# Kernel tuning notes

Hardware: AMD Instinct MI355X
Metric: run time of the kernel (lower is better)

Reference implementation:

```python
import jax, jax.numpy as jnp
import numpy as np

B, S, HID = 8, 1024, 1024
NH, HD = 16, 64  # num heads, head dim; NH*HD == HID


def setup_inputs() -> dict:
    key = jax.random.key(0)
    ks = jax.random.split(key, 8)
    sc = 0.02
    return {
        "hidden_states": jax.random.normal(ks[0], (B, S, HID), jnp.float32),
        "attention_mask": jnp.zeros((B, 1, 1, S), jnp.float32),
        "Wq": jax.random.normal(ks[1], (HID, HID), jnp.float32) * sc,
        "bq": jnp.zeros((HID,), jnp.float32),
        "Wk": jax.random.normal(ks[2], (HID, HID), jnp.float32) * sc,
        "bk": jnp.zeros((HID,), jnp.float32),
        "Wv": jax.random.normal(ks[3], (HID, HID), jnp.float32) * sc,
        "bv": jnp.zeros((HID,), jnp.float32),
    }


def reference(hidden_states, attention_mask, Wq, bq, Wk, bk, Wv, bv):
    def split_heads(x):  # [B,S,HID] -> [B,NH,S,HD]
        return x.reshape(B, S, NH, HD).transpose(0, 2, 1, 3)

    q = split_heads(hidden_states @ Wq + bq)
    k = split_heads(hidden_states @ Wk + bk)
    v = split_heads(hidden_states @ Wv + bv)

    # [B,NH,S,S] score matrix, scale, additive mask, softmax
    scores = jnp.einsum("bhqd,bhkd->bhqk", q, k) / jnp.sqrt(jnp.float32(HD))
    scores = scores + attention_mask
    probs = jax.nn.softmax(scores, axis=-1)  # dropout prob = 0.0 -> identity

    ctx = jnp.einsum("bhqk,bhkd->bhqd", probs, v)
    return ctx.transpose(0, 2, 1, 3).reshape(B, S, HID)
```

## Files before the change

### kernel.cpp

```cpp
#include <hip/hip_runtime.h>


typedef __bf16 bf16x8 __attribute__((ext_vector_type(8)));
typedef float f32x4 __attribute__((ext_vector_type(4)));
typedef float f32x16 __attribute__((ext_vector_type(16)));

__device__ __forceinline__ unsigned rne16(float x) {
  unsigned u = __builtin_bit_cast(unsigned, x);
  return (u + 0x7fffu + ((u >> 16) & 1u)) >> 16;
}
__device__ __forceinline__ unsigned packbf(float lo, float hi) {
  return rne16(lo) | (rne16(hi) << 16);
}
__device__ __forceinline__ unsigned packbf_fast(float lo, float hi) {
  unsigned ul = __builtin_bit_cast(unsigned, lo) + 0x8000u;
  unsigned uh = __builtin_bit_cast(unsigned, hi) + 0x8000u;
  return __builtin_amdgcn_perm(uh, ul, 0x07060302u);
}
__device__ __forceinline__ void async16(void* l, const void* g) {
  __builtin_amdgcn_global_load_lds((const __attribute__((address_space(1))) void*)g,
                                   (__attribute__((address_space(3))) void*)l, 16, 0, 0);
}

__global__ __launch_bounds__(256) void k_prep(const float* __restrict__ h,
                                              unsigned short* __restrict__ hbf,
                                              const float* __restrict__ Wq,
                                              const float* __restrict__ Wk,
                                              const float* __restrict__ Wv,
                                              unsigned short* __restrict__ wt) {
  __shared__ float t[32][33];
  int bid = blockIdx.x, tid = threadIdx.x;
  if (bid < 8192) {
    size_t i = (size_t)bid * 256 + tid;
    float4 v = ((const float4*)h)[i];
    uint2 r;
    r.x = packbf(v.x, v.y);
    r.y = packbf(v.z, v.w);
    ((uint2*)hbf)[i] = r;
  } else {
    int id = bid - 8192;
    int which = id >> 10;
    int sub = id & 1023;
    int c0 = (sub & 31) * 32, k0 = (sub >> 5) * 32;
    const float* W = which == 0 ? Wq : (which == 1 ? Wk : Wv);
    int tx = tid & 31, ty = tid >> 5;
#pragma unroll
    for (int i = 0; i < 4; ++i) {
      int r = ty + i * 8;
      t[r][tx] = W[(size_t)(k0 + r) * 1024 + c0 + tx];
    }
    __syncthreads();
#pragma unroll
    for (int i = 0; i < 4; ++i) {
      int r = ty + i * 8;
      wt[((size_t)which * 1024 + c0 + r) * 1024 + k0 + tx] = (unsigned short)rne16(t[tx][r]);
    }
  }
}

__global__ __launch_bounds__(256, 2) void k_gemm(const unsigned short* __restrict__ A,
                                                 const unsigned short* __restrict__ Bm,
                                                 const float* __restrict__ bq,
                                                 const float* __restrict__ bk,
                                                 const float* __restrict__ bv,
                                                 unsigned short* __restrict__ qkv,
                                                 unsigned short* __restrict__ vt) {
  __shared__ __align__(16) char lds[65536];
  const int tid = threadIdx.x;
  const int w = tid >> 6, lane = tid & 63;
  const int wm = w >> 1, wn = w & 1;

  int orig = blockIdx.x;
  int wgid = (orig & 7) * 192 + (orig >> 3);
  int tm = wgid / 24, tn = wgid - tm * 24;
  int m0 = tm * 128, n0 = tn * 128;

  int ro[4], ke[4];
#pragma unroll
  for (int j = 0; j < 4; ++j) {
    int o = j * 4096 + tid * 16;
    int s = o >> 10, w10 = o & 1023;
    int lg = w10 ^ (((w10 >> 9) & 1) << 5);
    ro[j] = ((s >> 1) << 4) + (lg >> 6);
    ke[j] = ((s & 1) << 5) + ((lg & 63) >> 1);
  }
  auto stage = [&](int kt, char* buf) {
    const unsigned short* As = A + (size_t)m0 * 1024 + kt * 64;
    const unsigned short* Bs = Bm + (size_t)n0 * 1024 + kt * 64;
#pragma unroll
    for (int j = 0; j < 4; ++j) {
      async16(buf + j * 4096 + tid * 16, As + (size_t)ro[j] * 1024 + ke[j]);
      async16(buf + 16384 + j * 4096 + tid * 16, Bs + (size_t)ro[j] * 1024 + ke[j]);
    }
  };

  const int lswz = (((lane & 15) << 6) | ((lane >> 4) << 4)) ^ ((lane & 8) << 2);

  f32x4 acc[4][4];
#pragma unroll
  for (int i = 0; i < 4; ++i)
#pragma unroll
    for (int j = 0; j < 4; ++j)
#pragma unroll
      for (int e = 0; e < 4; ++e) acc[i][j][e] = 0.f;

  auto compute = [&](const char* buf) {
    const char* abase = buf + lswz;
    const char* bbase = buf + 16384 + lswz;
#pragma unroll
    for (int ks = 0; ks < 2; ++ks) {
      bf16x8 bF[4];
#pragma unroll
      for (int n = 0; n < 4; ++n)
        bF[n] = *(const bf16x8*)(bbase + ((size_t)((wn * 4 + n) * 2 + ks) << 10));
#pragma unroll
      for (int mt = 0; mt < 4; ++mt) {
        bf16x8 a = *(const bf16x8*)(abase + ((size_t)((wm * 4 + mt) * 2 + ks) << 10));
#pragma unroll
        for (int n = 0; n < 4; ++n)
          acc[mt][n] =
              __builtin_amdgcn_mfma_f32_16x16x32_bf16(a, bF[n], acc[mt][n], 0, 0, 0);
      }
    }
  };

  char* buf0 = lds;
  char* buf1 = lds + 32768;
  stage(0, buf0);
#pragma unroll 1
  for (int kt = 0; kt < 16; kt += 2) {
    __syncthreads();
    stage(kt + 1, buf1);
    compute(buf0);
    __syncthreads();
    if (kt + 2 < 16) stage(kt + 2, buf0);
    compute(buf1);
  }

  const int which = tn >> 3;
  const int ng = n0 & 1023;
  const int b = m0 >> 10;
  const int r = lane & 15, qq = lane >> 4;
  const int sb = (m0 & 1023) + wm * 64 + qq * 4;

  if (which != 2) {
    const float* bp = which == 0 ? bq : bk;
    unsigned short* base = qkv + ((size_t)which << 23) + ((size_t)b << 20);
#pragma unroll
    for (int n = 0; n < 4; ++n) {
      int n_in = ng + wn * 64 + n * 16 + r;
      float bias = bp[n_in];
      unsigned short* dp = base + ((size_t)(n_in >> 6) << 16) + (n_in & 63);
#pragma unroll
      for (int m = 0; m < 4; ++m)
#pragma unroll
        for (int e = 0; e < 4; ++e)
          dp[(size_t)(sb + m * 16 + e) << 6] = (unsigned short)rne16(acc[m][n][e] + bias);
    }
  } else {
    unsigned short* vbase = vt + ((size_t)b << 20);
#pragma unroll
    for (int n = 0; n < 4; ++n) {
      int n_in = ng + wn * 64 + n * 16 + r;
      float bias = bv[n_in];
      unsigned short* dp = vbase + ((size_t)n_in << 10) + sb;
#pragma unroll
      for (int m = 0; m < 4; ++m) {
        uint2 pk;
        pk.x = packbf(acc[m][n][0] + bias, acc[m][n][1] + bias);
        pk.y = packbf(acc[m][n][2] + bias, acc[m][n][3] + bias);
        *(uint2*)(dp + m * 16) = pk;
      }
    }
  }
}

__global__ __launch_bounds__(256, 2) void k_attn(const unsigned short* __restrict__ qg,
                                                 const unsigned short* __restrict__ kg,
                                                 const unsigned short* __restrict__ vtg,
                                                 const float* __restrict__ maskg,
                                                 float* __restrict__ out) {
  __shared__ __align__(16) char lds[36864];
  float* MK = (float*)(lds + 32768);
  int tid = threadIdx.x, w = tid >> 6, lane = tid & 63, l5 = lane & 31, q5 = lane >> 5;
  int idx = blockIdx.x;
  int bi = idx & 7;
  int j = idx >> 3;
  int h = j >> 2, qc = j & 3;
  int bh = bi * 16 + h, s0 = qc * 256;
  const unsigned short* qb = qg + ((size_t)bh << 16);
  const unsigned short* kb = kg + ((size_t)bh << 16);
  const unsigned short* vb = vtg + ((size_t)bh << 16);
  const float LG = 1.4426950408889634f;
  const float C1 = 0.125f * LG;

  {
    float4 mv = *(const float4*)(maskg + (size_t)bi * 1024 + tid * 4);
    mv.x *= LG; mv.y *= LG; mv.z *= LG; mv.w *= LG;
    *(float4*)(MK + tid * 4) = mv;
  }

  auto stageKV = [&](int kt, char* buf) {
    int k0 = kt * 64;
#pragma unroll
    for (int t = 0; t < 2; ++t) {
      int f = w * 2 + t;
      int mt = f >> 2, ds = f & 3;
      async16(buf + f * 1024, kb + (size_t)(k0 + mt * 32 + l5) * 64 + ds * 16 + q5 * 8);
      int dt = f >> 2, ks = f & 3;
      async16(buf + 8192 + f * 1024,
              vb + (size_t)(dt * 32 + l5) * 1024 + k0 + ks * 16 + q5 * 8);
    }
  };

  bf16x8 qfr[2][4];
#pragma unroll
  for (int qh = 0; qh < 2; ++qh)
#pragma unroll
    for (int ds = 0; ds < 4; ++ds)
      qfr[qh][ds] = *(const bf16x8*)(qb + (size_t)(s0 + w * 64 + qh * 32 + l5) * 64 +
                                     ds * 16 + q5 * 8);

  f32x16 O[2][2];
#pragma unroll
  for (int qh = 0; qh < 2; ++qh)
#pragma unroll
    for (int i = 0; i < 2; ++i)
#pragma unroll
      for (int e = 0; e < 16; ++e) O[qh][i][e] = 0.f;
  float lsum0 = 0.f, lsum1 = 0.f;

  stageKV(0, lds);
  __syncthreads();

#pragma unroll 1
  for (int kt = 0; kt < 16; ++kt) {
    char* buf = lds + (kt & 1) * 16384;
    if (kt < 15) stageKV(kt + 1, lds + ((kt + 1) & 1) * 16384);
    int k0 = kt * 64;
    const char* KF = buf;
    const char* VF = buf + 8192;
#pragma unroll
    for (int mt = 0; mt < 2; ++mt) {
      f32x16 S0, S1;
#pragma unroll
      for (int e = 0; e < 16; ++e) { S0[e] = 0.f; S1[e] = 0.f; }
#pragma unroll
      for (int ds = 0; ds < 4; ++ds) {
        bf16x8 a = *(const bf16x8*)(KF + (mt * 4 + ds) * 1024 + lane * 16);
        S0 = __builtin_amdgcn_mfma_f32_32x32x16_bf16(a, qfr[0][ds], S0, 0, 0, 0);
        S1 = __builtin_amdgcn_mfma_f32_32x32x16_bf16(a, qfr[1][ds], S1, 0, 0, 0);
      }
      unsigned p2a[8], p2b[8];
      {
        float p[16];
#pragma unroll
        for (int g4 = 0; g4 < 4; ++g4) {
          float4 mv = *(const float4*)(MK + k0 + mt * 32 + g4 * 8 + q5 * 4);
          p[g4 * 4 + 0] = __builtin_amdgcn_exp2f(S0[g4 * 4 + 0] * C1 + mv.x);
          p[g4 * 4 + 1] = __builtin_amdgcn_exp2f(S0[g4 * 4 + 1] * C1 + mv.y);
          p[g4 * 4 + 2] = __builtin_amdgcn_exp2f(S0[g4 * 4 + 2] * C1 + mv.z);
          p[g4 * 4 + 3] = __builtin_amdgcn_exp2f(S0[g4 * 4 + 3] * C1 + mv.w);
        }
#pragma unroll
        for (int e = 0; e < 16; ++e) lsum0 += p[e];
#pragma unroll
        for (int jj = 0; jj < 8; ++jj) p2a[jj] = packbf_fast(p[2 * jj], p[2 * jj + 1]);
      }
      {
        float p[16];
#pragma unroll
        for (int g4 = 0; g4 < 4; ++g4) {
          float4 mv = *(const float4*)(MK + k0 + mt * 32 + g4 * 8 + q5 * 4);
          p[g4 * 4 + 0] = __builtin_amdgcn_exp2f(S1[g4 * 4 + 0] * C1 + mv.x);
          p[g4 * 4 + 1] = __builtin_amdgcn_exp2f(S1[g4 * 4 + 1] * C1 + mv.y);
          p[g4 * 4 + 2] = __builtin_amdgcn_exp2f(S1[g4 * 4 + 2] * C1 + mv.z);
          p[g4 * 4 + 3] = __builtin_amdgcn_exp2f(S1[g4 * 4 + 3] * C1 + mv.w);
        }
#pragma unroll
        for (int e = 0; e < 16; ++e) lsum1 += p[e];
#pragma unroll
        for (int jj = 0; jj < 8; ++jj) p2b[jj] = packbf_fast(p[2 * jj], p[2 * jj + 1]);
      }
#pragma unroll
      for (int kh = 0; kh < 2; ++kh) {
        int ks = mt * 2 + kh, gp = kh * 4;
        bf16x8 av0 = *(const bf16x8*)(VF + (0 * 4 + ks) * 1024 + lane * 16);
        bf16x8 av1 = *(const bf16x8*)(VF + (1 * 4 + ks) * 1024 + lane * 16);
        {
          unsigned o0 = p2a[gp + 0], o1 = p2a[gp + 1];
          unsigned o2 = p2a[gp + 2], o3 = p2a[gp + 3];
          unsigned t0 = __shfl_xor((int)o0, 32);
          unsigned t1 = __shfl_xor((int)o1, 32);
          unsigned t2 = __shfl_xor((int)o2, 32);
          unsigned t3 = __shfl_xor((int)o3, 32);
          uint4 fu;
          fu.x = q5 ? t2 : o0;
          fu.y = q5 ? t3 : o1;
          fu.z = q5 ? o2 : t0;
          fu.w = q5 ? o3 : t1;
          bf16x8 bfrag = __builtin_bit_cast(bf16x8, fu);
          O[0][0] = __builtin_amdgcn_mfma_f32_32x32x16_bf16(av0, bfrag, O[0][0], 0, 0, 0);
          O[0][1] = __builtin_amdgcn_mfma_f32_32x32x16_bf16(av1, bfrag, O[0][1], 0, 0, 0);
        }
        {
          unsigned o0 = p2b[gp + 0], o1 = p2b[gp + 1];
          unsigned o2 = p2b[gp + 2], o3 = p2b[gp + 3];
          unsigned t0 = __shfl_xor((int)o0, 32);
          unsigned t1 = __shfl_xor((int)o1, 32);
          unsigned t2 = __shfl_xor((int)o2, 32);
          unsigned t3 = __shfl_xor((int)o3, 32);
          uint4 fu;
          fu.x = q5 ? t2 : o0;
          fu.y = q5 ? t3 : o1;
          fu.z = q5 ? o2 : t0;
          fu.w = q5 ? o3 : t1;
          bf16x8 bfrag = __builtin_bit_cast(bf16x8, fu);
          O[1][0] = __builtin_amdgcn_mfma_f32_32x32x16_bf16(av0, bfrag, O[1][0], 0, 0, 0);
          O[1][1] = __builtin_amdgcn_mfma_f32_32x32x16_bf16(av1, bfrag, O[1][1], 0, 0, 0);
        }
      }
    }
    __syncthreads();
  }

  float* Ob = (float*)(lds + w * 8192);
  float lt0 = lsum0 + __shfl_xor(lsum0, 32);
  float lt1 = lsum1 + __shfl_xor(lsum1, 32);
  float rinv0 = 1.0f / lt0;
  float rinv1 = 1.0f / lt1;
#pragma unroll
  for (int qh = 0; qh < 2; ++qh) {
    float rinv = qh ? rinv1 : rinv0;
#pragma unroll
    for (int dt = 0; dt < 2; ++dt)
#pragma unroll
      for (int g4 = 0; g4 < 4; ++g4) {
        float4 val;
        val.x = O[qh][dt][g4 * 4 + 0] * rinv;
        val.y = O[qh][dt][g4 * 4 + 1] * rinv;
        val.z = O[qh][dt][g4 * 4 + 2] * rinv;
        val.w = O[qh][dt][g4 * 4 + 3] * rinv;
        int c = dt * 8 + g4 * 2 + q5;
        *(float4*)(Ob + l5 * 64 + (c ^ (l5 & 15)) * 4) = val;
      }
#pragma unroll
    for (int t = 0; t < 8; ++t) {
      int qr = t * 4 + (lane >> 4), cr = lane & 15;
      float4 vv = *(const float4*)(Ob + qr * 64 + (cr ^ (qr & 15)) * 4);
      int s = s0 + w * 64 + qh * 32 + qr;
      *(float4*)(out + (((size_t)(bi * 1024 + s)) << 10) + (h << 6) + (cr << 2)) = vv;
    }
  }
}

extern "C" void kernel_launch(void* const* d_in, const int* in_sizes, int n_in,
                              void* d_out, int out_size, void* d_ws, size_t ws_size,
                              hipStream_t stream) {
  (void)in_sizes; (void)n_in; (void)out_size; (void)ws_size;
  const float* hidden = (const float*)d_in[0];
  const float* mask = (const float*)d_in[1];
  const float* Wq = (const float*)d_in[2];
  const float* bq = (const float*)d_in[3];
  const float* Wk = (const float*)d_in[4];
  const float* bk = (const float*)d_in[5];
  const float* Wv = (const float*)d_in[6];
  const float* bv = (const float*)d_in[7];
  float* out = (float*)d_out;
  char* ws = (char*)d_ws;
  unsigned short* hbf = (unsigned short*)ws;
  unsigned short* wt  = (unsigned short*)(ws + 16777216);
  unsigned short* qkv = (unsigned short*)(ws + 23068672);
  unsigned short* vt  = (unsigned short*)(ws + 56623104);

  k_prep<<<11264, 256, 0, stream>>>(hidden, hbf, Wq, Wk, Wv, wt);
  k_gemm<<<1536, 256, 0, stream>>>(hbf, wt, bq, bk, bv, qkv, vt);
  k_attn<<<512, 256, 0, stream>>>(qkv, qkv + 8388608, vt, mask, out);
}
```

Measured before the change: 209.0 us.

## Widen QKV GEMM tiles to 128x384 with half-depth K stages

Reshapes the fused QKV projection GEMM from 128x128 tiles to 128x384 tiles, so each workgroup covers three times as many output columns and reuses its A tile across them. The K step per stage is halved to 32 so the LDS buffers still fit, and the grid drops from 1536 to 512 workgroups. Each wave now holds 48 accumulator fragments, which raises register pressure and may force spills or lower occupancy. The smaller grid also gives fewer workgroups per CU for hiding latency.

```diff
diff --git a/kernel.cpp b/kernel.cpp
--- a/kernel.cpp
+++ b/kernel.cpp
@@ -71,56 +71,54 @@
   const int wm = w >> 1, wn = w & 1;
 
   int orig = blockIdx.x;
-  int wgid = (orig & 7) * 192 + (orig >> 3);
-  int tm = wgid / 24, tn = wgid - tm * 24;
-  int m0 = tm * 128, n0 = tn * 128;
-
-  int ro[4], ke[4];
-#pragma unroll
-  for (int j = 0; j < 4; ++j) {
+  int wgid = (orig & 7) * 64 + (orig >> 3);
+  int tm = wgid >> 3, tn = wgid & 7;
+  int m0 = tm * 128, n0 = tn * 384;
+
+  int ro[6], ke[6];
+#pragma unroll
+  for (int j = 0; j < 6; ++j) {
     int o = j * 4096 + tid * 16;
     int s = o >> 10, w10 = o & 1023;
     int lg = w10 ^ (((w10 >> 9) & 1) << 5);
-    ro[j] = ((s >> 1) << 4) + (lg >> 6);
-    ke[j] = ((s & 1) << 5) + ((lg & 63) >> 1);
+    ro[j] = s * 16 + (lg >> 6);
+    ke[j] = (lg & 63) >> 1;
   }
   auto stage = [&](int kt, char* buf) {
-    const unsigned short* As = A + (size_t)m0 * 1024 + kt * 64;
-    const unsigned short* Bs = Bm + (size_t)n0 * 1024 + kt * 64;
-#pragma unroll
-    for (int j = 0; j < 4; ++j) {
+    const unsigned short* As = A + (size_t)m0 * 1024 + kt * 32;
+    const unsigned short* Bs = Bm + (size_t)n0 * 1024 + kt * 32;
+#pragma unroll
+    for (int j = 0; j < 2; ++j)
       async16(buf + j * 4096 + tid * 16, As + (size_t)ro[j] * 1024 + ke[j]);
-      async16(buf + 16384 + j * 4096 + tid * 16, Bs + (size_t)ro[j] * 1024 + ke[j]);
-    }
+#pragma unroll
+    for (int j = 0; j < 6; ++j)
+      async16(buf + 8192 + j * 4096 + tid * 16, Bs + (size_t)ro[j] * 1024 + ke[j]);
   };
 
   const int lswz = (((lane & 15) << 6) | ((lane >> 4) << 4)) ^ ((lane & 8) << 2);
 
-  f32x4 acc[4][4];
+  f32x4 acc[4][12];
 #pragma unroll
   for (int i = 0; i < 4; ++i)
 #pragma unroll
-    for (int j = 0; j < 4; ++j)
+    for (int j = 0; j < 12; ++j)
 #pragma unroll
       for (int e = 0; e < 4; ++e) acc[i][j][e] = 0.f;
 
   auto compute = [&](const char* buf) {
     const char* abase = buf + lswz;
-    const char* bbase = buf + 16384 + lswz;
-#pragma unroll
-    for (int ks = 0; ks < 2; ++ks) {
-      bf16x8 bF[4];
-#pragma unroll
-      for (int n = 0; n < 4; ++n)
-        bF[n] = *(const bf16x8*)(bbase + ((size_t)((wn * 4 + n) * 2 + ks) << 10));
-#pragma unroll
-      for (int mt = 0; mt < 4; ++mt) {
-        bf16x8 a = *(const bf16x8*)(abase + ((size_t)((wm * 4 + mt) * 2 + ks) << 10));
-#pragma unroll
-        for (int n = 0; n < 4; ++n)
-          acc[mt][n] =
-              __builtin_amdgcn_mfma_f32_16x16x32_bf16(a, bF[n], acc[mt][n], 0, 0, 0);
-      }
+    const char* bbase = buf + 8192 + lswz;
+    bf16x8 aF[4];
+#pragma unroll
+    for (int mt = 0; mt < 4; ++mt)
+      aF[mt] = *(const bf16x8*)(abase + ((size_t)(wm * 4 + mt) << 10));
+#pragma unroll
+    for (int n = 0; n < 12; ++n) {
+      bf16x8 bF = *(const bf16x8*)(bbase + ((size_t)(wn * 12 + n) << 10));
+#pragma unroll
+      for (int mt = 0; mt < 4; ++mt)
+        acc[mt][n] =
+            __builtin_amdgcn_mfma_f32_16x16x32_bf16(aF[mt], bF, acc[mt][n], 0, 0, 0);
     }
   };
 
@@ -128,42 +126,36 @@
   char* buf1 = lds + 32768;
   stage(0, buf0);
 #pragma unroll 1
-  for (int kt = 0; kt < 16; kt += 2) {
+  for (int kt = 0; kt < 32; kt += 2) {
     __syncthreads();
     stage(kt + 1, buf1);
     compute(buf0);
     __syncthreads();
-    if (kt + 2 < 16) stage(kt + 2, buf0);
+    if (kt + 2 < 32) stage(kt + 2, buf0);
     compute(buf1);
   }
 
-  const int which = tn >> 3;
-  const int ng = n0 & 1023;
   const int b = m0 >> 10;
   const int r = lane & 15, qq = lane >> 4;
   const int sb = (m0 & 1023) + wm * 64 + qq * 4;
-
-  if (which != 2) {
-    const float* bp = which == 0 ? bq : bk;
-    unsigned short* base = qkv + ((size_t)which << 23) + ((size_t)b << 20);
-#pragma unroll
-    for (int n = 0; n < 4; ++n) {
-      int n_in = ng + wn * 64 + n * 16 + r;
+#pragma unroll
+  for (int n = 0; n < 12; ++n) {
+    int n_gf = n0 + wn * 192 + n * 16;
+    int which = n_gf >> 10;
+    int n_in = (n_gf & 1023) + r;
+    if (which != 2) {
+      const float* bp = which == 0 ? bq : bk;
       float bias = bp[n_in];
-      unsigned short* dp = base + ((size_t)(n_in >> 6) << 16) + (n_in & 63);
+      unsigned short* dp = qkv + ((size_t)which << 23) + ((size_t)b << 20) +
+                           ((size_t)(n_in >> 6) << 16) + (n_in & 63);
 #pragma unroll
       for (int m = 0; m < 4; ++m)
 #pragma unroll
         for (int e = 0; e < 4; ++e)
           dp[(size_t)(sb + m * 16 + e) << 6] = (unsigned short)rne16(acc[m][n][e] + bias);
-    }
-  } else {
-    unsigned short* vbase = vt + ((size_t)b << 20);
-#pragma unroll
-    for (int n = 0; n < 4; ++n) {
-      int n_in = ng + wn * 64 + n * 16 + r;
+    } else {
       float bias = bv[n_in];
-      unsigned short* dp = vbase + ((size_t)n_in << 10) + sb;
+      unsigned short* dp = vt + ((size_t)b << 20) + ((size_t)n_in << 10) + sb;
 #pragma unroll
       for (int m = 0; m < 4; ++m) {
         uint2 pk;
@@ -374,6 +366,6 @@
   unsigned short* vt  = (unsigned short*)(ws + 56623104);
 
   k_prep<<<11264, 256, 0, stream>>>(hidden, hbf, Wq, Wk, Wv, wt);
-  k_gemm<<<1536, 256, 0, stream>>>(hbf, wt, bq, bk, bv, qkv, vt);
+  k_gemm<<<512, 256, 0, stream>>>(hbf, wt, bq, bk, bv, qkv, vt);
   k_attn<<<512, 256, 0, stream>>>(qkv, qkv + 8388608, vt, mask, out);
 }
```

Result: no change. 210.3 us (+0.6%).
